# Kernel optimization log

Measured on AMD Instinct MI355X. Metric: run time of the kernel, lower is better.

Reference implementation:

```python
import jax, jax.numpy as jnp
import numpy as np

N = 50000
E = 800000
IN_CH = 128
HID = 64
HEADS = 4
G = 64  # number of graphs in batch
NEG_SLOPE = 0.2


def setup_inputs() -> dict:
    key = jax.random.key(0)
    ks = jax.random.split(key, 16)
    s = lambda fan_in: 1.0 / np.sqrt(fan_in)
    x = jax.random.normal(ks[0], (N, IN_CH), dtype=jnp.float32)
    edge_index = jax.random.randint(ks[1], (2, E), 0, N, dtype=jnp.int64)
    batch = jnp.sort(jax.random.randint(ks[2], (N,), 0, G, dtype=jnp.int64))
    # GAT layer 1: in 128 -> heads*hid = 256
    W1 = jax.random.uniform(ks[3], (IN_CH, HEADS * HID), jnp.float32, -s(IN_CH), s(IN_CH))
    a1_src = jax.random.uniform(ks[4], (HEADS, HID), jnp.float32, -s(HID), s(HID))
    a1_dst = jax.random.uniform(ks[5], (HEADS, HID), jnp.float32, -s(HID), s(HID))
    b1 = jnp.zeros((HEADS * HID,), jnp.float32)
    # GAT layer 2: in 256 -> heads*hid = 256
    W2 = jax.random.uniform(ks[6], (HEADS * HID, HEADS * HID), jnp.float32, -s(HEADS * HID), s(HEADS * HID))
    a2_src = jax.random.uniform(ks[7], (HEADS, HID), jnp.float32, -s(HID), s(HID))
    a2_dst = jax.random.uniform(ks[8], (HEADS, HID), jnp.float32, -s(HID), s(HID))
    b2 = jnp.zeros((HEADS * HID,), jnp.float32)
    # post-pool MLP: (in + 2*heads*hid) -> 256 -> 128
    d_cat = IN_CH + 2 * HEADS * HID
    W3 = jax.random.uniform(ks[9], (d_cat, 256), jnp.float32, -s(d_cat), s(d_cat))
    b3 = jnp.zeros((256,), jnp.float32)
    W4 = jax.random.uniform(ks[10], (256, 128), jnp.float32, -s(256), s(256))
    b4 = jnp.zeros((128,), jnp.float32)
    return {"x": x, "edge_index": edge_index, "batch": batch,
            "W1": W1, "a1_src": a1_src, "a1_dst": a1_dst, "b1": b1,
            "W2": W2, "a2_src": a2_src, "a2_dst": a2_dst, "b2": b2,
            "W3": W3, "b3": b3, "W4": W4, "b4": b4}


def gat_layer(x, src, dst, W, a_src, a_dst, b):
    n = x.shape[0]
    h = (x @ W).reshape(n, HEADS, HID)                 # [N,H,D]
    e_src = jnp.einsum('nhd,hd->nh', h, a_src)         # [N,H]
    e_dst = jnp.einsum('nhd,hd->nh', h, a_dst)
    e = jax.nn.leaky_relu(e_src[src] + e_dst[dst], NEG_SLOPE)  # [E,H]
    # segment softmax over incoming edges of each destination node
    m = jax.ops.segment_max(e, dst, num_segments=n)
    m = jnp.where(jnp.isfinite(m), m, 0.0)
    ex = jnp.exp(e - m[dst])
    denom = jax.ops.segment_sum(ex, dst, num_segments=n)
    alpha = ex / (denom[dst] + 1e-16)                  # [E,H]
    msg = h[src] * alpha[:, :, None]                   # [E,H,D]
    out = jax.ops.segment_sum(msg, dst, num_segments=n)
    return out.reshape(n, HEADS * HID) + b


def reference(x, edge_index, batch, W1, a1_src, a1_dst, b1, W2, a2_src, a2_dst, b2, W3, b3, W4, b4):
    src, dst = edge_index[0], edge_index[1]
    h0 = x
    h1 = jax.nn.relu(gat_layer(h0, src, dst, W1, a1_src, a1_dst, b1))
    h2 = jax.nn.relu(gat_layer(h1, src, dst, W2, a2_src, a2_dst, b2))
    comb = jnp.concatenate([h0, h1, h2], axis=-1)      # [N, 128+256+256]
    sums = jax.ops.segment_sum(comb, batch, num_segments=G)
    cnt = jax.ops.segment_sum(jnp.ones((x.shape[0],), comb.dtype), batch, num_segments=G)
    pooled = sums / jnp.maximum(cnt, 1.0)[:, None]     # [G, 640]
    hmlp = jax.nn.relu(pooled @ W3 + b3)               # dropout is identity at eval
    return hmlp @ W4 + b4                              # [G, 128]
```

## Files before the change

kernel.cpp:

```cpp
#include <hip/hip_runtime.h>
#include <cstdint>
#include <cstddef>

#define N_NODES 50000
#define M_PAD 50048
#define E_EDGES 800000
#define INCH 128
#define HID 64
#define HEADS 4
#define NHD 256
#define NGRAPH 64
#define DCAT 640
#define NEG_SLOPE 0.2f

typedef __attribute__((ext_vector_type(8))) short bf16x8;
typedef __attribute__((ext_vector_type(4))) float f32x4;

static __device__ inline unsigned short f2bf(float f) {
    unsigned int u = __float_as_uint(f);
    unsigned int r = (u + 0x7FFFu + ((u >> 16) & 1u)) >> 16;
    return (unsigned short)r;
}
static __device__ inline float bf2f(unsigned short b) {
    return __uint_as_float(((unsigned int)b) << 16);
}

__global__ void wsplit_kernel(const float* __restrict__ W,
                              unsigned short* __restrict__ Wthi,
                              unsigned short* __restrict__ Wtlo, int K)
{
    const int i = blockIdx.x * 256 + threadIdx.x;
    if (i >= K * NHD) return;
    const int n = i / K, k = i - n * K;
    const float v = W[(size_t)k * NHD + n];
    const unsigned short hi = f2bf(v);
    Wthi[i] = hi;
    Wtlo[i] = f2bf(v - bf2f(hi));
}

__global__ void asplit_kernel(const float* __restrict__ A,
                              unsigned short* __restrict__ Ahi,
                              unsigned short* __restrict__ Alo, int n)
{
    const int i = blockIdx.x * 256 + threadIdx.x;
    if (i >= n) return;
    const float v = A[i];
    const unsigned short h = f2bf(v);
    Ahi[i] = h;
    Alo[i] = f2bf(v - bf2f(h));
}

#define GK 64
#define LDAB 72

__global__ __launch_bounds__(256, 2) void gemm_mfma(
    const unsigned short* __restrict__ Athi,
    const unsigned short* __restrict__ Atlo,
    const unsigned short* __restrict__ Bthi,
    const unsigned short* __restrict__ Btlo,
    const float* __restrict__ asrc, const float* __restrict__ adst,
    unsigned short* __restrict__ Cb, float* __restrict__ es,
    float* __restrict__ ed, int M, int K)
{
    __shared__ unsigned short Ahi[128 * LDAB];
    __shared__ unsigned short Alo[128 * LDAB];
    __shared__ unsigned short Bhi[128 * LDAB];
    __shared__ unsigned short Blo[128 * LDAB];

    const int t    = threadIdx.x;
    const int row0 = blockIdx.x * 128;
    const int col0 = blockIdx.y * 128;
    const int wave = t >> 6, lane = t & 63;
    const int wr = (wave >> 1) * 64;
    const int wc = (wave & 1) * 64;
    const int m16 = lane & 15, quad = lane >> 4;

    f32x4 acc[4][4];
#pragma unroll
    for (int i = 0; i < 4; ++i)
#pragma unroll
        for (int j = 0; j < 4; ++j) acc[i][j] = (f32x4){0.f, 0.f, 0.f, 0.f};

    for (int k0 = 0; k0 < K; k0 += GK) {
#pragma unroll
        for (int i = 0; i < 4; ++i) {
            const int seg = t + i * 256;
            const int r = seg >> 3, p = (seg & 7) * 8;
            const size_t ga = (size_t)(row0 + r) * K + k0 + p;
            const size_t gb = (size_t)(col0 + r) * K + k0 + p;
            *(int4*)(&Ahi[r * LDAB + p]) = *(const int4*)(Athi + ga);
            *(int4*)(&Alo[r * LDAB + p]) = *(const int4*)(Atlo + ga);
            *(int4*)(&Bhi[r * LDAB + p]) = *(const int4*)(Bthi + gb);
            *(int4*)(&Blo[r * LDAB + p]) = *(const int4*)(Btlo + gb);
        }
        __syncthreads();

#pragma unroll
        for (int h = 0; h < 2; ++h) {
            bf16x8 afh[4], afl[4], bfh[4], bfl[4];
#pragma unroll
            for (int i = 0; i < 4; ++i) {
                const int r = wr + i * 16 + m16;
                afh[i] = *(const bf16x8*)(&Ahi[r * LDAB + h * 32 + quad * 8]);
                afl[i] = *(const bf16x8*)(&Alo[r * LDAB + h * 32 + quad * 8]);
            }
#pragma unroll
            for (int j = 0; j < 4; ++j) {
                const int n = wc + j * 16 + m16;
                bfh[j] = *(const bf16x8*)(&Bhi[n * LDAB + h * 32 + quad * 8]);
                bfl[j] = *(const bf16x8*)(&Blo[n * LDAB + h * 32 + quad * 8]);
            }
#pragma unroll
            for (int i = 0; i < 4; ++i)
#pragma unroll
                for (int j = 0; j < 4; ++j) {
                    acc[i][j] = __builtin_amdgcn_mfma_f32_16x16x32_bf16(afh[i], bfh[j], acc[i][j], 0, 0, 0);
                    acc[i][j] = __builtin_amdgcn_mfma_f32_16x16x32_bf16(afh[i], bfl[j], acc[i][j], 0, 0, 0);
                    acc[i][j] = __builtin_amdgcn_mfma_f32_16x16x32_bf16(afl[i], bfh[j], acc[i][j], 0, 0, 0);
                }
        }
        __syncthreads();
    }

#pragma unroll
    for (int i = 0; i < 4; ++i)
#pragma unroll
        for (int reg = 0; reg < 4; ++reg) {
            const int r = row0 + wr + i * 16 + quad * 4 + reg;
            if (r < M) {
#pragma unroll
                for (int j = 0; j < 4; ++j)
                    Cb[(size_t)r * NHD + col0 + wc + j * 16 + m16] = f2bf(acc[i][j][reg]);
            }
        }

    const int head = (col0 + wc) >> 6;
    float a_s[4], a_d[4];
#pragma unroll
    for (int j = 0; j < 4; ++j) {
        a_s[j] = asrc[head * HID + j * 16 + m16];
        a_d[j] = adst[head * HID + j * 16 + m16];
    }
#pragma unroll
    for (int i = 0; i < 4; ++i)
#pragma unroll
        for (int reg = 0; reg < 4; ++reg) {
            float ps = 0.f, pd = 0.f;
#pragma unroll
            for (int j = 0; j < 4; ++j) {
                const float v = acc[i][j][reg];
                ps += v * a_s[j];
                pd += v * a_d[j];
            }
#pragma unroll
            for (int off = 1; off < 16; off <<= 1) {
                ps += __shfl_xor(ps, off, 64);
                pd += __shfl_xor(pd, off, 64);
            }
            if (m16 == 0) {
                const int r = row0 + wr + i * 16 + quad * 4 + reg;
                if (r < M) {
                    es[r * HEADS + head] = ps;
                    ed[r * HEADS + head] = pd;
                }
            }
        }
}

__global__ void hist_kernel(const int* __restrict__ ei, int* __restrict__ counts)
{
    const int e = blockIdx.x * 256 + threadIdx.x;
    if (e >= E_EDGES) return;
    atomicAdd(&counts[ei[E_EDGES + e]], 1);
}

#define SBLK 1024
#define NSCB ((N_NODES + SBLK - 1) / SBLK)

__global__ __launch_bounds__(1024) void scan_local_kernel(
    const int* __restrict__ counts, int* __restrict__ offsets,
    int* __restrict__ bsum)
{
    __shared__ int tmp[SBLK];
    const int t = threadIdx.x;
    const int i = blockIdx.x * SBLK + t;
    const int v = (i < N_NODES) ? counts[i] : 0;
    tmp[t] = v;
    __syncthreads();
    for (int off = 1; off < SBLK; off <<= 1) {
        const int u = (t >= off) ? tmp[t - off] : 0;
        __syncthreads();
        tmp[t] += u;
        __syncthreads();
    }
    if (i < N_NODES) offsets[i] = tmp[t] - v;
    if (t == SBLK - 1) bsum[blockIdx.x] = tmp[t];
}

__global__ __launch_bounds__(1024) void scan_final_kernel(
    int* __restrict__ offsets, int* __restrict__ cursor,
    const int* __restrict__ bsum)
{
    __shared__ int base_sh;
    const int b = blockIdx.x;
    if (threadIdx.x == 0) {
        int s = 0;
        for (int j = 0; j < b; ++j) s += bsum[j];
        base_sh = s;
    }
    __syncthreads();
    const int i = b * SBLK + threadIdx.x;
    if (i < N_NODES) {
        const int v = offsets[i] + base_sh;
        offsets[i] = v;
        cursor[i]  = v;
    }
    if (b == 0 && threadIdx.x == 0) offsets[N_NODES] = E_EDGES;
}

__global__ void scatter_kernel(const int* __restrict__ ei, int* __restrict__ cursor,
                               int* __restrict__ csr)
{
    const int e = blockIdx.x * 256 + threadIdx.x;
    if (e >= E_EDGES) return;
    const int d = ei[E_EDGES + e];
    const int pos = atomicAdd(&cursor[d], 1);
    csr[pos] = e;
}

__global__ __launch_bounds__(256) void aggregate_fused(
    const unsigned short* __restrict__ hb, const int* __restrict__ ei,
    const int* __restrict__ csr, const int* __restrict__ offsets,
    const float* __restrict__ es, const float* __restrict__ ed,
    const float* __restrict__ bias, unsigned short* __restrict__ outhi,
    unsigned short* __restrict__ outlo)
{
    const int wid  = threadIdx.x >> 6;
    const int lane = threadIdx.x & 63;
    const int node = blockIdx.x * 4 + wid;
    if (node >= N_NODES) return;
    const int head = lane >> 4;
    const int col  = lane * 4;
    const int sub  = lane & 15;

    const float edc = ed[node * 4 + head];
    const int beg = offsets[node], end = offsets[node + 1];

    float4 acc = make_float4(0.f, 0.f, 0.f, 0.f);
    float dsum = 0.f;

    int base = beg;
    int m_cur = min(16, end - base);
    int s_cur = 0; float w_cur = 0.f;
    if (base < end && sub < m_cur) {
        const int eid = csr[base + sub];
        s_cur = ei[eid];
        float u = es[s_cur * 4 + head] + edc;
        u = u > 0.f ? u : NEG_SLOPE * u;
        w_cur = expf(u);
    }

    while (base < end) {
        const int base_n = base + 16;
        const int m_nxt = min(16, end - base_n);
        int s_nxt = 0; float w_nxt = 0.f;
        if (base_n < end && sub < m_nxt) {
            const int eid = csr[base_n + sub];
            s_nxt = ei[eid];
            float u = es[s_nxt * 4 + head] + edc;
            u = u > 0.f ? u : NEG_SLOPE * u;
            w_nxt = expf(u);
        }
        if (m_cur == 16) {
#pragma unroll
            for (int i = 0; i < 16; ++i) {
                const int   s = (int)__builtin_amdgcn_readlane((unsigned)s_cur, i);
                const float w = __shfl(w_cur, (lane & 48) + i, 64);
                const ushort4 v = *(const ushort4*)(hb + (size_t)s * NHD + col);
                acc.x += w * bf2f(v.x);
                acc.y += w * bf2f(v.y);
                acc.z += w * bf2f(v.z);
                acc.w += w * bf2f(v.w);
                dsum += w;
            }
        } else {
            for (int i = 0; i < m_cur; ++i) {
                const int   s = __shfl(s_cur, i, 64);
                const float w = __shfl(w_cur, (lane & 48) + i, 64);
                const ushort4 v = *(const ushort4*)(hb + (size_t)s * NHD + col);
                acc.x += w * bf2f(v.x);
                acc.y += w * bf2f(v.y);
                acc.z += w * bf2f(v.z);
                acc.w += w * bf2f(v.w);
                dsum += w;
            }
        }
        s_cur = s_nxt; w_cur = w_nxt; m_cur = m_nxt; base = base_n;
    }

    const float inv = 1.0f / (dsum + 1e-16f);
    const float4 bb = *(const float4*)(bias + col);
    float4 o;
    o.x = fmaxf(acc.x * inv + bb.x, 0.f);
    o.y = fmaxf(acc.y * inv + bb.y, 0.f);
    o.z = fmaxf(acc.z * inv + bb.z, 0.f);
    o.w = fmaxf(acc.w * inv + bb.w, 0.f);
    ushort4 oh;
    oh.x = f2bf(o.x); oh.y = f2bf(o.y); oh.z = f2bf(o.z); oh.w = f2bf(o.w);
    *(ushort4*)(outhi + (size_t)node * NHD + col) = oh;
    if (outlo) {
        ushort4 ol;
        ol.x = f2bf(o.x - bf2f(oh.x));
        ol.y = f2bf(o.y - bf2f(oh.y));
        ol.z = f2bf(o.z - bf2f(oh.z));
        ol.w = f2bf(o.w - bf2f(oh.w));
        *(ushort4*)(outlo + (size_t)node * NHD + col) = ol;
    }
}

__global__ void graph_offsets_kernel(const int* __restrict__ batch, int* __restrict__ goff)
{
    const int n = blockIdx.x * 256 + threadIdx.x;
    if (n >= N_NODES) return;
    const int b  = batch[n];
    const int bp = (n == 0) ? -1 : batch[n - 1];
    for (int g = bp + 1; g <= b; ++g) goff[g] = n;
    if (n == N_NODES - 1) {
        for (int g = b + 1; g <= NGRAPH; ++g) goff[g] = N_NODES;
    }
}

#define PRB 128

__global__ __launch_bounds__(640) void pool_sum_kernel(
    const float* __restrict__ x, const unsigned short* __restrict__ h1b,
    const unsigned short* __restrict__ h2b, const int* __restrict__ batch,
    float* __restrict__ sums)
{
    __shared__ int bsh[PRB];
    const int c  = threadIdx.x;
    const int r0 = blockIdx.x * PRB;
    const int r1 = min(N_NODES, r0 + PRB);
    const int nr = r1 - r0;
    if (c < nr) bsh[c] = batch[r0 + c];
    __syncthreads();

    const float* srcf = nullptr;
    const unsigned short* srcb = nullptr;
    int ld, cc;
    if (c < INCH)            { srcf = x;   ld = INCH; cc = c; }
    else if (c < INCH + NHD) { srcb = h1b; ld = NHD;  cc = c - INCH; }
    else                     { srcb = h2b; ld = NHD;  cc = c - INCH - NHD; }

    float sum = 0.f;
    int g = bsh[0];
    for (int i = 0; i < nr; ++i) {
        const int gb = bsh[i];
        if (gb != g) {
            atomicAdd(&sums[g * DCAT + c], sum);
            sum = 0.f;
            g = gb;
        }
        sum += srcf ? srcf[(size_t)(r0 + i) * ld + cc]
                    : bf2f(srcb[(size_t)(r0 + i) * ld + cc]);
    }
    atomicAdd(&sums[g * DCAT + c], sum);
}

__global__ void pool_finalize_kernel(const float* __restrict__ sums,
                                     const int* __restrict__ goff,
                                     float* __restrict__ pooled)
{
    const int i = blockIdx.x * 256 + threadIdx.x;
    if (i >= NGRAPH * DCAT) return;
    const int g = i / DCAT;
    const float cnt = (float)(goff[g + 1] - goff[g]);
    pooled[i] = sums[i] / fmaxf(cnt, 1.0f);
}

__global__ __launch_bounds__(256) void mlp_kernel(
    const float* __restrict__ pooled, const float* __restrict__ W3,
    const float* __restrict__ b3, const float* __restrict__ W4,
    const float* __restrict__ b4, float* __restrict__ out)
{
    const int g = blockIdx.x;
    __shared__ float p[DCAT];
    __shared__ float hm[256];
    for (int i = threadIdx.x; i < DCAT; i += 256) p[i] = pooled[(size_t)g * DCAT + i];
    __syncthreads();
    float s = b3[threadIdx.x];
    for (int k = 0; k < DCAT; ++k) s += p[k] * W3[(size_t)k * 256 + threadIdx.x];
    hm[threadIdx.x] = fmaxf(s, 0.f);
    __syncthreads();
    if (threadIdx.x < 128) {
        float o = b4[threadIdx.x];
        for (int k = 0; k < 256; ++k) o += hm[k] * W4[(size_t)k * 128 + threadIdx.x];
        out[(size_t)g * 128 + threadIdx.x] = o;
    }
}

extern "C" void kernel_launch(void* const* d_in, const int* in_sizes, int n_in,
                              void* d_out, int out_size, void* d_ws, size_t ws_size,
                              hipStream_t stream)
{
    const float* x     = (const float*)d_in[0];
    const int*   ei    = (const int*)d_in[1];
    const int*   batch = (const int*)d_in[2];
    const float* W1    = (const float*)d_in[3];
    const float* a1s   = (const float*)d_in[4];
    const float* a1d   = (const float*)d_in[5];
    const float* b1    = (const float*)d_in[6];
    const float* W2    = (const float*)d_in[7];
    const float* a2s   = (const float*)d_in[8];
    const float* a2d   = (const float*)d_in[9];
    const float* b2    = (const float*)d_in[10];
    const float* W3    = (const float*)d_in[11];
    const float* b3    = (const float*)d_in[12];
    const float* W4    = (const float*)d_in[13];
    const float* b4    = (const float*)d_in[14];
    float* out = (float*)d_out;

    size_t off = 0;
    auto carve = [&](size_t bytes) -> void* {
        void* p = (char*)d_ws + off;
        off = (off + bytes + 255) & ~(size_t)255;
        return p;
    };
    unsigned short* xhi   = (unsigned short*)carve((size_t)M_PAD * INCH * 2);
    unsigned short* xlo   = (unsigned short*)carve((size_t)M_PAD * INCH * 2);
    unsigned short* ghi   = (unsigned short*)carve((size_t)N_NODES * NHD * 2);
    unsigned short* h1hi  = (unsigned short*)carve((size_t)M_PAD * NHD * 2);
    unsigned short* h1lo  = (unsigned short*)carve((size_t)M_PAD * NHD * 2);
    unsigned short* h2hi  = (unsigned short*)carve((size_t)N_NODES * NHD * 2);
    float* es     = (float*)carve((size_t)N_NODES * HEADS * 4);
    float* ed     = (float*)carve((size_t)N_NODES * HEADS * 4);
    float* pooled = (float*)carve((size_t)NGRAPH * DCAT * 4);
    float* psums  = (float*)carve((size_t)NGRAPH * DCAT * 4);
    int*   counts  = (int*)carve((size_t)N_NODES * 4);
    int*   offsets = (int*)carve((size_t)(N_NODES + 1) * 4);
    int*   cursor  = (int*)carve((size_t)N_NODES * 4);
    int*   csr     = (int*)carve((size_t)E_EDGES * 4);
    int*   goff    = (int*)carve((size_t)(NGRAPH + 1) * 4);
    int*   bsum    = (int*)carve((size_t)NSCB * 4);
    unsigned short* w1thi = (unsigned short*)carve((size_t)NHD * INCH * 2);
    unsigned short* w1tlo = (unsigned short*)carve((size_t)NHD * INCH * 2);
    unsigned short* w2thi = (unsigned short*)carve((size_t)NHD * NHD * 2);
    unsigned short* w2tlo = (unsigned short*)carve((size_t)NHD * NHD * 2);

    const int egrid = (E_EDGES + 255) / 256;
    const int ngrid = (N_NODES + 255) / 256;

    hipMemsetAsync(counts, 0, (size_t)N_NODES * 4, stream);
    hist_kernel<<<egrid, 256, 0, stream>>>(ei, counts);
    scan_local_kernel<<<NSCB, SBLK, 0, stream>>>(counts, offsets, bsum);
    scan_final_kernel<<<NSCB, SBLK, 0, stream>>>(offsets, cursor, bsum);
    scatter_kernel<<<egrid, 256, 0, stream>>>(ei, cursor, csr);
    graph_offsets_kernel<<<ngrid, 256, 0, stream>>>(batch, goff);
    wsplit_kernel<<<(INCH * NHD + 255) / 256, 256, 0, stream>>>(W1, w1thi, w1tlo, INCH);
    wsplit_kernel<<<(NHD * NHD + 255) / 256, 256, 0, stream>>>(W2, w2thi, w2tlo, NHD);
    asplit_kernel<<<(N_NODES * INCH + 255) / 256, 256, 0, stream>>>(x, xhi, xlo, N_NODES * INCH);

    dim3 ggrid((M_PAD + 127) / 128, NHD / 128);

    gemm_mfma<<<ggrid, 256, 0, stream>>>(xhi, xlo, w1thi, w1tlo, a1s, a1d,
                                         ghi, es, ed, N_NODES, INCH);
    aggregate_fused<<<(N_NODES + 3) / 4, 256, 0, stream>>>(ghi, ei, csr, offsets,
                                                           es, ed, b1, h1hi, h1lo);
    gemm_mfma<<<ggrid, 256, 0, stream>>>(h1hi, h1lo, w2thi, w2tlo, a2s, a2d,
                                         ghi, es, ed, N_NODES, NHD);
    aggregate_fused<<<(N_NODES + 3) / 4, 256, 0, stream>>>(ghi, ei, csr, offsets,
                                                           es, ed, b2, h2hi, nullptr);

    hipMemsetAsync(psums, 0, (size_t)NGRAPH * DCAT * 4, stream);
    pool_sum_kernel<<<(N_NODES + PRB - 1) / PRB, 640, 0, stream>>>(x, h1hi, h2hi, batch, psums);
    pool_finalize_kernel<<<(NGRAPH * DCAT + 255) / 256, 256, 0, stream>>>(psums, goff, pooled);
    mlp_kernel<<<NGRAPH, 256, 0, stream>>>(pooled, W3, b3, W4, b4, out);
}
```

Before: 504.0 us.

## Widen aggregation gathers to 16B with two edges per wave, fuse small kernels

The aggregation kernel now splits each wave into two halves that each process a different edge per iteration. Each lane gathers 8 bf16 values (16 bytes) instead of 4, and the two halves are combined with a cross-half shuffle at the end. The change also merges the three weight/x split kernels into one launch and folds pool finalization into the MLP kernel, which removes several launches and a buffer. In exchange it adds shuffle work, masked partial tail iterations and more registers per lane.

Result: faster. 493.3 us (-2.1%).

```diff
diff --git a/kernel.cpp b/kernel.cpp
--- a/kernel.cpp
+++ b/kernel.cpp
@@ -25,29 +25,33 @@
     return __uint_as_float(((unsigned int)b) << 16);
 }
 
-__global__ void wsplit_kernel(const float* __restrict__ W,
-                              unsigned short* __restrict__ Wthi,
-                              unsigned short* __restrict__ Wtlo, int K)
+#define W1N (INCH * NHD)
+#define W2N (NHD * NHD)
+#define XN  (N_NODES * INCH)
+__global__ void split_all_kernel(
+    const float* __restrict__ W1, const float* __restrict__ W2,
+    const float* __restrict__ x,
+    unsigned short* __restrict__ w1thi, unsigned short* __restrict__ w1tlo,
+    unsigned short* __restrict__ w2thi, unsigned short* __restrict__ w2tlo,
+    unsigned short* __restrict__ xhi, unsigned short* __restrict__ xlo)
 {
     const int i = blockIdx.x * 256 + threadIdx.x;
-    if (i >= K * NHD) return;
-    const int n = i / K, k = i - n * K;
-    const float v = W[(size_t)k * NHD + n];
-    const unsigned short hi = f2bf(v);
-    Wthi[i] = hi;
-    Wtlo[i] = f2bf(v - bf2f(hi));
-}
-
-__global__ void asplit_kernel(const float* __restrict__ A,
-                              unsigned short* __restrict__ Ahi,
-                              unsigned short* __restrict__ Alo, int n)
-{
-    const int i = blockIdx.x * 256 + threadIdx.x;
-    if (i >= n) return;
-    const float v = A[i];
+    float v; unsigned short* dhi; unsigned short* dlo; int idx;
+    if (i < W1N) {
+        const int n = i / INCH, k = i - n * INCH;
+        v = W1[(size_t)k * NHD + n]; dhi = w1thi; dlo = w1tlo; idx = i;
+    } else if (i < W1N + W2N) {
+        const int j = i - W1N;
+        const int n = j / NHD, k = j - n * NHD;
+        v = W2[(size_t)k * NHD + n]; dhi = w2thi; dlo = w2tlo; idx = j;
+    } else {
+        const int j = i - W1N - W2N;
+        if (j >= XN) return;
+        v = x[j]; dhi = xhi; dlo = xlo; idx = j;
+    }
     const unsigned short h = f2bf(v);
-    Ahi[i] = h;
-    Alo[i] = f2bf(v - bf2f(h));
+    dhi[idx] = h;
+    dlo[idx] = f2bf(v - bf2f(h));
 }
 
 #define GK 64
@@ -239,14 +243,19 @@
     const int lane = threadIdx.x & 63;
     const int node = blockIdx.x * 4 + wid;
     if (node >= N_NODES) return;
-    const int head = lane >> 4;
-    const int col  = lane * 4;
-    const int sub  = lane & 15;
-
-    const float edc = ed[node * 4 + head];
+    const int head_p = lane >> 4;
+    const int sub    = lane & 15;
+    const int half   = lane >> 5;
+    const int hl     = lane & 31;
+    const int col8   = hl * 8;
+    const int widx   = (hl >> 3) << 4;
+
+    const float edc = ed[node * 4 + head_p];
     const int beg = offsets[node], end = offsets[node + 1];
 
-    float4 acc = make_float4(0.f, 0.f, 0.f, 0.f);
+    float acc[8];
+#pragma unroll
+    for (int k = 0; k < 8; ++k) acc[k] = 0.f;
     float dsum = 0.f;
 
     int base = beg;
@@ -255,7 +264,7 @@
     if (base < end && sub < m_cur) {
         const int eid = csr[base + sub];
         s_cur = ei[eid];
-        float u = es[s_cur * 4 + head] + edc;
+        float u = es[s_cur * 4 + head_p] + edc;
         u = u > 0.f ? u : NEG_SLOPE * u;
         w_cur = expf(u);
     }
@@ -267,54 +276,66 @@
         if (base_n < end && sub < m_nxt) {
             const int eid = csr[base_n + sub];
             s_nxt = ei[eid];
-            float u = es[s_nxt * 4 + head] + edc;
+            float u = es[s_nxt * 4 + head_p] + edc;
             u = u > 0.f ? u : NEG_SLOPE * u;
             w_nxt = expf(u);
         }
         if (m_cur == 16) {
 #pragma unroll
-            for (int i = 0; i < 16; ++i) {
-                const int   s = (int)__builtin_amdgcn_readlane((unsigned)s_cur, i);
-                const float w = __shfl(w_cur, (lane & 48) + i, 64);
-                const ushort4 v = *(const ushort4*)(hb + (size_t)s * NHD + col);
-                acc.x += w * bf2f(v.x);
-                acc.y += w * bf2f(v.y);
-                acc.z += w * bf2f(v.z);
-                acc.w += w * bf2f(v.w);
+            for (int i = 0; i < 16; i += 2) {
+                const int e0 = i + half;
+                const int   s = __shfl(s_cur, e0, 64);
+                const float w = __shfl(w_cur, widx + e0, 64);
+                const bf16x8 v = *(const bf16x8*)(hb + (size_t)s * NHD + col8);
+#pragma unroll
+                for (int k = 0; k < 8; ++k)
+                    acc[k] += w * bf2f((unsigned short)v[k]);
                 dsum += w;
             }
         } else {
-            for (int i = 0; i < m_cur; ++i) {
-                const int   s = __shfl(s_cur, i, 64);
-                const float w = __shfl(w_cur, (lane & 48) + i, 64);
-                const ushort4 v = *(const ushort4*)(hb + (size_t)s * NHD + col);
-                acc.x += w * bf2f(v.x);
-                acc.y += w * bf2f(v.y);
-                acc.z += w * bf2f(v.z);
-                acc.w += w * bf2f(v.w);
-                dsum += w;
+            for (int i = 0; i < m_cur; i += 2) {
+                const int e0 = i + half;
+                const int   s = __shfl(s_cur, e0 & 15, 64);
+                const float w = __shfl(w_cur, widx + (e0 & 15), 64);
+                const bf16x8 v = *(const bf16x8*)(hb + (size_t)s * NHD + col8);
+                const float we = (e0 < m_cur) ? w : 0.f;
+#pragma unroll
+                for (int k = 0; k < 8; ++k)
+                    acc[k] += we * bf2f((unsigned short)v[k]);
+                dsum += we;
             }
         }
         s_cur = s_nxt; w_cur = w_nxt; m_cur = m_nxt; base = base_n;
     }
 
+    dsum += __shfl_xor(dsum, 32, 64);
+#pragma unroll
+    for (int k = 0; k < 8; ++k) acc[k] += __shfl_xor(acc[k], 32, 64);
+
     const float inv = 1.0f / (dsum + 1e-16f);
-    const float4 bb = *(const float4*)(bias + col);
-    float4 o;
-    o.x = fmaxf(acc.x * inv + bb.x, 0.f);
-    o.y = fmaxf(acc.y * inv + bb.y, 0.f);
-    o.z = fmaxf(acc.z * inv + bb.z, 0.f);
-    o.w = fmaxf(acc.w * inv + bb.w, 0.f);
-    ushort4 oh;
-    oh.x = f2bf(o.x); oh.y = f2bf(o.y); oh.z = f2bf(o.z); oh.w = f2bf(o.w);
-    *(ushort4*)(outhi + (size_t)node * NHD + col) = oh;
-    if (outlo) {
-        ushort4 ol;
-        ol.x = f2bf(o.x - bf2f(oh.x));
-        ol.y = f2bf(o.y - bf2f(oh.y));
-        ol.z = f2bf(o.z - bf2f(oh.z));
-        ol.w = f2bf(o.w - bf2f(oh.w));
-        *(ushort4*)(outlo + (size_t)node * NHD + col) = ol;
+    const float4 bb0 = *(const float4*)(bias + col8);
+    const float4 bb1 = *(const float4*)(bias + col8 + 4);
+    float o[8];
+    o[0] = fmaxf(acc[0] * inv + bb0.x, 0.f);
+    o[1] = fmaxf(acc[1] * inv + bb0.y, 0.f);
+    o[2] = fmaxf(acc[2] * inv + bb0.z, 0.f);
+    o[3] = fmaxf(acc[3] * inv + bb0.w, 0.f);
+    o[4] = fmaxf(acc[4] * inv + bb1.x, 0.f);
+    o[5] = fmaxf(acc[5] * inv + bb1.y, 0.f);
+    o[6] = fmaxf(acc[6] * inv + bb1.z, 0.f);
+    o[7] = fmaxf(acc[7] * inv + bb1.w, 0.f);
+
+    bf16x8 hi8;
+#pragma unroll
+    for (int k = 0; k < 8; ++k) hi8[k] = (short)f2bf(o[k]);
+    if (half == 0) {
+        *(bf16x8*)(outhi + (size_t)node * NHD + col8) = hi8;
+    } else if (outlo) {
+        bf16x8 lo8;
+#pragma unroll
+        for (int k = 0; k < 8; ++k)
+            lo8[k] = (short)f2bf(o[k] - bf2f((unsigned short)hi8[k]));
+        *(bf16x8*)(outlo + (size_t)node * NHD + col8) = lo8;
     }
 }
 
@@ -367,26 +388,18 @@
     atomicAdd(&sums[g * DCAT + c], sum);
 }
 
-__global__ void pool_finalize_kernel(const float* __restrict__ sums,
-                                     const int* __restrict__ goff,
-                                     float* __restrict__ pooled)
-{
-    const int i = blockIdx.x * 256 + threadIdx.x;
-    if (i >= NGRAPH * DCAT) return;
-    const int g = i / DCAT;
-    const float cnt = (float)(goff[g + 1] - goff[g]);
-    pooled[i] = sums[i] / fmaxf(cnt, 1.0f);
-}
-
 __global__ __launch_bounds__(256) void mlp_kernel(
-    const float* __restrict__ pooled, const float* __restrict__ W3,
-    const float* __restrict__ b3, const float* __restrict__ W4,
-    const float* __restrict__ b4, float* __restrict__ out)
+    const float* __restrict__ psums, const int* __restrict__ goff,
+    const float* __restrict__ W3, const float* __restrict__ b3,
+    const float* __restrict__ W4, const float* __restrict__ b4,
+    float* __restrict__ out)
 {
     const int g = blockIdx.x;
     __shared__ float p[DCAT];
     __shared__ float hm[256];
-    for (int i = threadIdx.x; i < DCAT; i += 256) p[i] = pooled[(size_t)g * DCAT + i];
+    const float inv = 1.0f / fmaxf((float)(goff[g + 1] - goff[g]), 1.0f);
+    for (int i = threadIdx.x; i < DCAT; i += 256)
+        p[i] = psums[(size_t)g * DCAT + i] * inv;
     __syncthreads();
     float s = b3[threadIdx.x];
     for (int k = 0; k < DCAT; ++k) s += p[k] * W3[(size_t)k * 256 + threadIdx.x];
@@ -434,7 +447,6 @@
     unsigned short* h2hi  = (unsigned short*)carve((size_t)N_NODES * NHD * 2);
     float* es     = (float*)carve((size_t)N_NODES * HEADS * 4);
     float* ed     = (float*)carve((size_t)N_NODES * HEADS * 4);
-    float* pooled = (float*)carve((size_t)NGRAPH * DCAT * 4);
     float* psums  = (float*)carve((size_t)NGRAPH * DCAT * 4);
     int*   counts  = (int*)carve((size_t)N_NODES * 4);
     int*   offsets = (int*)carve((size_t)(N_NODES + 1) * 4);
@@ -456,9 +468,8 @@
     scan_final_kernel<<<NSCB, SBLK, 0, stream>>>(offsets, cursor, bsum);
     scatter_kernel<<<egrid, 256, 0, stream>>>(ei, cursor, csr);
     graph_offsets_kernel<<<ngrid, 256, 0, stream>>>(batch, goff);
-    wsplit_kernel<<<(INCH * NHD + 255) / 256, 256, 0, stream>>>(W1, w1thi, w1tlo, INCH);
-    wsplit_kernel<<<(NHD * NHD + 255) / 256, 256, 0, stream>>>(W2, w2thi, w2tlo, NHD);
-    asplit_kernel<<<(N_NODES * INCH + 255) / 256, 256, 0, stream>>>(x, xhi, xlo, N_NODES * INCH);
+    split_all_kernel<<<(W1N + W2N + XN + 255) / 256, 256, 0, stream>>>(
+        W1, W2, x, w1thi, w1tlo, w2thi, w2tlo, xhi, xlo);
 
     dim3 ggrid((M_PAD + 127) / 128, NHD / 128);
 
@@ -473,6 +484,5 @@
 
     hipMemsetAsync(psums, 0, (size_t)NGRAPH * DCAT * 4, stream);
     pool_sum_kernel<<<(N_NODES + PRB - 1) / PRB, 640, 0, stream>>>(x, h1hi, h2hi, batch, psums);
-    pool_finalize_kernel<<<(NGRAPH * DCAT + 255) / 256, 256, 0, stream>>>(psums, goff, pooled);
-    mlp_kernel<<<NGRAPH, 256, 0, stream>>>(pooled, W3, b3, W4, b4, out);
-}
+    mlp_kernel<<<NGRAPH, 256, 0, stream>>>(psums, goff, W3, b3, W4, b4, out);
+}
```
